# Kernel tuning notes

Measured on AMD Instinct MI355X. Metric: run time of the kernel, lower is better.

Reference implementation:

```python
import jax, jax.numpy as jnp
import numpy as np

VOCAB = 100000
E = 256      # embedding dim == projection dim (required by layer-axis concat)
H = 2048     # lstm hidden dim
P = 256      # projection dim
B, T = 8, 96
CELL_CLIP = 3.0
PROJ_CLIP = 3.0
NUM_LAYERS = 2


def setup_inputs() -> dict:
    key = jax.random.key(0)
    ks = jax.random.split(key, 8)
    tokens = jax.random.randint(ks[0], (B, T), 0, VOCAB, dtype=jnp.int32)
    mask = jnp.ones((B, T, 1), dtype=jnp.float32)
    embed_table = jax.random.normal(ks[1], (VOCAB + 1, E), dtype=jnp.float32) * 0.05
    # stacked LSTM weights: index 0=fwd L0, 1=fwd L1, 2=bwd L0, 3=bwd L1
    Wk = jax.random.normal(ks[2], (4, E, 4 * H), dtype=jnp.float32) * 0.02
    Wr = jax.random.normal(ks[3], (4, P, 4 * H), dtype=jnp.float32) * 0.02
    b = jnp.zeros((4, 4 * H), dtype=jnp.float32)
    Wp = jax.random.normal(ks[4], (4, H, P), dtype=jnp.float32) * 0.02
    elmo_w = jnp.zeros((NUM_LAYERS + 1,), dtype=jnp.float32)
    gamma = jnp.ones((1,), dtype=jnp.float32)
    return {"tokens": tokens, "mask": mask, "embed_table": embed_table,
            "Wk": Wk, "Wr": Wr, "b": b, "Wp": Wp,
            "elmo_w": elmo_w, "gamma": gamma}


def _lstm_proj(x, m, Wk, Wr, b, Wp, reverse):
    # x: [B,T,E], m: [B,T,1]. LSTM with cell clip, output projection, proj clip.
    if reverse:
        x = jnp.flip(x, 1)
        m = jnp.flip(m, 1)
    xs = jnp.swapaxes(x, 0, 1)                     # [T,B,E]
    ms = jnp.swapaxes(m, 0, 1)                     # [T,B,1]
    xW = jnp.einsum('tbe,ef->tbf', xs, Wk) + b     # precompute input gates [T,B,4H]

    def step(carry, inp):
        h, c = carry                               # h:[B,P], c:[B,H]
        zx, mt = inp
        z = zx + h @ Wr                            # [B,4H]
        i, f, g, o = jnp.split(z, 4, axis=-1)
        i = jax.nn.sigmoid(i)
        f = jax.nn.sigmoid(f)
        g = jnp.tanh(g)
        o = jax.nn.sigmoid(o)
        c_new = jnp.clip(f * c + i * g, -CELL_CLIP, CELL_CLIP)
        h_new = jnp.clip((o * jnp.tanh(c_new)) @ Wp, -PROJ_CLIP, PROJ_CLIP)
        keep = mt > 0
        h_new = jnp.where(keep, h_new, h)
        c_new = jnp.where(keep, c_new, c)
        return (h_new, c_new), h_new

    h0 = jnp.zeros((x.shape[0], Wp.shape[1]), x.dtype)
    c0 = jnp.zeros((x.shape[0], Wp.shape[0]), x.dtype)
    _, hs = jax.lax.scan(step, (h0, c0), (xW, ms))
    out = jnp.swapaxes(hs, 0, 1)                   # [B,T,P]
    if reverse:
        out = jnp.flip(out, 1)
    return out


def _elmo_layers(tokens, mask, embed_table, Wk, Wr, b, Wp):
    emb = embed_table[tokens]                      # [B,T,E]
    dir_outs = []
    for rev, base in ((False, 0), (True, 2)):
        inp = emb
        outs = []
        for l in range(NUM_LAYERS):
            out = _lstm_proj(inp, mask, Wk[base + l], Wr[base + l],
                             b[base + l], Wp[base + l], rev)
            inp = inp + out if l > 0 else out      # skip connection on layer > 0
            outs.append(inp)
        dir_outs.append(outs)
    fwd, bwd = dir_outs
    layers = [jnp.concatenate([emb, emb], -1)]
    layers += [jnp.concatenate([f, bb], -1) for f, bb in zip(fwd, bwd)]
    return jnp.stack(layers, axis=1)               # [B, L+1, T, 2P]


def reference(tokens, mask, embed_table, Wk, Wr, b, Wp, elmo_w, gamma):
    all_emb = _elmo_layers(tokens, mask, embed_table, Wk, Wr, b, Wp)
    m = mask[:, None, :, :]                        # [B,1,T,1]
    num = jnp.sum(mask, axis=(1, 2))[:, None]      # [B,1]
    xm = all_emb * m
    mean = jnp.sum(xm, axis=(2, 3)) / num          # [B,L+1]
    mean = mean[:, :, None, None]
    var = jnp.sum(((xm - mean) * m) ** 2, axis=(2, 3)) / num
    var = var[:, :, None, None]
    normed = (all_emb - mean) / jnp.sqrt(var + 1e-12)
    w = jax.nn.softmax(elmo_w)[None, :, None, None]
    weighted = jnp.sum(w * normed, axis=1) * gamma  # [B,T,2P]
    return weighted
```

## Files before the change

kernel.cpp:

```cpp
#include <hip/hip_runtime.h>
#include <hip/hip_bf16.h>

#define DEVFN __device__ __forceinline__

static constexpr size_t OFF_CTRS   = 0;
static constexpr size_t OFF_STATS  = 131328;
static constexpr size_t OFF_EW     = 131584;
static constexpr size_t OFF_MASK32 = 131840;
static constexpr size_t OFF_EMB    = 135168;
static constexpr size_t OFF_WPT    = 921600;
static constexpr size_t OFF_BIAS   = 9310208;
static constexpr size_t OFF_XW     = 9441280;
static constexpr size_t OFF_OUT0   = 59772928;
static constexpr size_t OFF_OUT1   = 61345792;
static constexpr size_t OFF_Y      = 62918656;
static constexpr size_t OFF_H      = 75501568;

template<int BF>
DEVFN float ldin(const void* p, size_t i) {
  if (BF) {
    unsigned short u = ((const unsigned short*)p)[i];
    return __uint_as_float(((unsigned)u) << 16);
  }
  return ((const float*)p)[i];
}
DEVFN float ldraw(const void* p, size_t i, int bf) {
  if (bf) {
    unsigned short u = ((const unsigned short*)p)[i];
    return __uint_as_float(((unsigned)u) << 16);
  }
  return ((const float*)p)[i];
}

DEVFN float sigm(float x) { return 1.f / (1.f + __expf(-x)); }
DEVFN float clip3(float x) { return fminf(fmaxf(x, -3.f), 3.f); }

DEVFN int detect_bf(const void* maskp) {
  return (((const unsigned*)maskp)[0] == 0x3F800000u) ? 0 : 1;
}

template<int BF>
__global__ void prep_k(const int* __restrict__ tokens, const void* __restrict__ maskp,
                       const void* __restrict__ et, const void* __restrict__ bias,
                       const void* __restrict__ ew, const void* __restrict__ gm,
                       const void* __restrict__ Wp,
                       float* bias32, float* mask32, float* ew32, float* emb, float* WpT) {
  if (detect_bf(maskp) != BF) return;
  const int bid = blockIdx.x, tid = threadIdx.x;

  if (bid < 132) {
    size_t i = (size_t)bid * 256 + tid;
    if (i >= 33540) return;
    if (i < 32768)       bias32[i] = ldin<BF>(bias, i);
    else if (i < 33536)  mask32[i - 32768] = ldin<BF>(maskp, i - 32768);
    else if (i < 33539)  ew32[i - 33536]   = ldin<BF>(ew, i - 33536);
    else                 ew32[3] = ldin<BF>(gm, 0);
    return;
  }

  if (bid < 644) {
    const int r = bid - 132;
    const int kt = r & 31, pt = (r >> 5) & 3, dl = r >> 7;
    __shared__ float tile[64][65];
    for (int it = 0; it < 4; ++it) {
      int lin = it * 1024 + tid * 4;
      int kk = lin >> 6, pp = lin & 63;
      size_t src = ((size_t)(dl * 2048 + kt * 64 + kk)) * 256 + pt * 64 + pp;
      float v0, v1, v2, v3;
      if (BF) {
        const unsigned short* sp = (const unsigned short*)Wp + src;
        v0 = __uint_as_float(((unsigned)sp[0]) << 16);
        v1 = __uint_as_float(((unsigned)sp[1]) << 16);
        v2 = __uint_as_float(((unsigned)sp[2]) << 16);
        v3 = __uint_as_float(((unsigned)sp[3]) << 16);
      } else {
        float4 v = *(const float4*)((const float*)Wp + src);
        v0 = v.x; v1 = v.y; v2 = v.z; v3 = v.w;
      }
      tile[pp + 0][kk] = v0; tile[pp + 1][kk] = v1; tile[pp + 2][kk] = v2; tile[pp + 3][kk] = v3;
    }
    __syncthreads();
    for (int it = 0; it < 4; ++it) {
      int lin = it * 1024 + tid * 4;
      int pr = lin >> 6, kc = lin & 63;
      float4 o;
      o.x = tile[pr][kc + 0]; o.y = tile[pr][kc + 1]; o.z = tile[pr][kc + 2]; o.w = tile[pr][kc + 3];
      *(float4*)(WpT + ((size_t)(dl * 256 + pt * 64 + pr)) * 2048 + kt * 64 + kc) = o;
    }
    return;
  }

  const int bt = bid - 644;
  const int tok = tokens[bt];
  emb[(size_t)bt * 256 + tid] = ldin<BF>(et, (size_t)tok * 256 + tid);
}

template<int BF>
__global__ __launch_bounds__(256) void xw_gemm_k(
    const void* __restrict__ maskp, const float* __restrict__ x_fwd, const float* __restrict__ x_bwd,
    const void* __restrict__ Wk, const float* __restrict__ bias32, float* __restrict__ xW, int layer) {
  if (detect_bf(maskp) != BF) return;
  const int nt = blockIdx.x, mt = blockIdx.y, dir = blockIdx.z;
  const int dl = dir * 2 + layer;
  const float* xb = dir ? x_bwd : x_fwd;
  const int tid = threadIdx.x;

  __shared__ float As[16][68];
  __shared__ float Bs[16][68];

  float acc[4][4] = {};
  const int tx = tid & 15, ty = tid >> 4;

  const int am = tid >> 2;
  const int ak = (tid & 3) * 4;
  const int m_glob = mt * 64 + am;
  const int t_ = m_glob >> 3, b_ = m_glob & 7;
  const int tau = dir ? (95 - t_) : t_;
  const float* arow = xb + ((size_t)(b_ * 96 + tau)) * 256;

  const int bk = tid >> 4, bn = (tid & 15) * 4;

  for (int kb = 0; kb < 256; kb += 16) {
    float4 av = *(const float4*)(arow + kb + ak);
    As[ak + 0][am] = av.x; As[ak + 1][am] = av.y; As[ak + 2][am] = av.z; As[ak + 3][am] = av.w;

    size_t bidx = ((size_t)dl * 256 + (kb + bk)) * 8192 + (size_t)nt * 64 + bn;
    float b0, b1, b2, b3;
    if (BF) {
      ushort4 uv = *(const ushort4*)((const unsigned short*)Wk + bidx);
      b0 = __uint_as_float(((unsigned)uv.x) << 16);
      b1 = __uint_as_float(((unsigned)uv.y) << 16);
      b2 = __uint_as_float(((unsigned)uv.z) << 16);
      b3 = __uint_as_float(((unsigned)uv.w) << 16);
    } else {
      float4 fv = *(const float4*)((const float*)Wk + bidx);
      b0 = fv.x; b1 = fv.y; b2 = fv.z; b3 = fv.w;
    }
    Bs[bk][bn + 0] = b0; Bs[bk][bn + 1] = b1; Bs[bk][bn + 2] = b2; Bs[bk][bn + 3] = b3;
    __syncthreads();

#pragma unroll
    for (int kk = 0; kk < 16; ++kk) {
      float a0 = As[kk][ty * 4 + 0], a1 = As[kk][ty * 4 + 1], a2 = As[kk][ty * 4 + 2], a3 = As[kk][ty * 4 + 3];
      float c0 = Bs[kk][tx * 4 + 0], c1 = Bs[kk][tx * 4 + 1], c2 = Bs[kk][tx * 4 + 2], c3 = Bs[kk][tx * 4 + 3];
      acc[0][0] = fmaf(a0, c0, acc[0][0]); acc[0][1] = fmaf(a0, c1, acc[0][1]);
      acc[0][2] = fmaf(a0, c2, acc[0][2]); acc[0][3] = fmaf(a0, c3, acc[0][3]);
      acc[1][0] = fmaf(a1, c0, acc[1][0]); acc[1][1] = fmaf(a1, c1, acc[1][1]);
      acc[1][2] = fmaf(a1, c2, acc[1][2]); acc[1][3] = fmaf(a1, c3, acc[1][3]);
      acc[2][0] = fmaf(a2, c0, acc[2][0]); acc[2][1] = fmaf(a2, c1, acc[2][1]);
      acc[2][2] = fmaf(a2, c2, acc[2][2]); acc[2][3] = fmaf(a2, c3, acc[2][3]);
      acc[3][0] = fmaf(a3, c0, acc[3][0]); acc[3][1] = fmaf(a3, c1, acc[3][1]);
      acc[3][2] = fmaf(a3, c2, acc[3][2]); acc[3][3] = fmaf(a3, c3, acc[3][3]);
    }
    __syncthreads();
  }

  const int n0 = nt * 64 + tx * 4;
#pragma unroll
  for (int i = 0; i < 4; ++i) {
    int m = mt * 64 + ty * 4 + i;
    int tt = m >> 3, bb = m & 7;
    float4 o;
    o.x = acc[i][0] + bias32[dl * 8192 + n0 + 0];
    o.y = acc[i][1] + bias32[dl * 8192 + n0 + 1];
    o.z = acc[i][2] + bias32[dl * 8192 + n0 + 2];
    o.w = acc[i][3] + bias32[dl * 8192 + n0 + 3];
    *(float4*)(xW + (size_t)((dir * 96 + tt) * 8 + bb) * 8192 + n0) = o;
  }
}


__global__ __launch_bounds__(256, 2) void scan_kernel(
    const float* __restrict__ xW, const void* __restrict__ WrRaw, const void* __restrict__ maskp,
    const float* __restrict__ WpT, const float* __restrict__ mask32,
    float* __restrict__ out, float* __restrict__ hbuf, float* __restrict__ ybuf,
    int* ctrs, int layer) {
  const int tid = threadIdx.x;
  const int w = blockIdx.x;
  const int dir = w >> 8;
  const int g = w & 255;
  const int dl = dir * 2 + layer;

  __shared__ __align__(16) float wr_s[256 * 32];
  __shared__ __align__(16) float h_lds[2048];
  __shared__ float4 wp4_s[512];
  __shared__ float4 zpart[288];
  __shared__ float  z_s[32 * 9];
  __shared__ __align__(16) float xw_s[256];
  __shared__ float  mask_s[768];
  __shared__ float  c_s[64];
  __shared__ float  red_s[8];

  int* base   = ctrs + (layer * 2 + dir) * 4096;
  int* aline  = base + (g >> 2) * 64;
  int* myline = base + (tid & 63) * 64;
  int ep = 0;
  const int bf = detect_bf(maskp);

  {
    const size_t wrbase = (size_t)dl * 256 * 8192;
    for (int i = tid; i < 8192; i += 256) {
      int k = i >> 5, col = i & 31;
      wr_s[i] = ldraw(WrRaw, wrbase + (size_t)k * 8192 + (size_t)(col >> 3) * 2048 + g * 8 + (col & 7), bf);
    }
    const float4* wrow = (const float4*)(WpT + ((size_t)(dl * 256 + g)) * 2048);
    for (int i = tid; i < 512; i += 256) wp4_s[i] = wrow[i];
    for (int i = tid; i < 768; i += 256) mask_s[i] = mask32[i];
  }
  if (tid < 64) c_s[tid] = 0.f;

  const int ks = tid >> 6, colq = (tid >> 3) & 7, lb = tid & 7;
  const float4* wr4 = (const float4*)wr_s;
  const float4* xw4 = (const float4*)xw_s;
  const int pb = tid >> 5, pcol = tid & 31;

  float xwv = xW[(size_t)((dir * 96 + 0) * 8 + pb) * 8192 + (pcol >> 3) * 2048 + g * 8 + (pcol & 7)];

  for (int t = 0; t < 96; ++t) {
    const int tau = dir ? (95 - t) : t;
    const float* h_cur = hbuf + ((size_t)(t * 2 + dir)) * 2048;
    float* h_nxt = hbuf + ((size_t)((t + 1) * 2 + dir)) * 2048;
    float* y_t   = ybuf + ((size_t)(t * 2 + dir)) * 16384;

    if (t == 0) {
      ((float4*)h_lds)[tid * 2 + 0] = make_float4(0.f, 0.f, 0.f, 0.f);
      ((float4*)h_lds)[tid * 2 + 1] = make_float4(0.f, 0.f, 0.f, 0.f);
    } else {
      ((float4*)h_lds)[tid * 2 + 0] = ((const float4*)h_cur)[tid * 2 + 0];
      ((float4*)h_lds)[tid * 2 + 1] = ((const float4*)h_cur)[tid * 2 + 1];
    }
    __syncthreads();

    {
      float4 acc = make_float4(0.f, 0.f, 0.f, 0.f);
#pragma unroll 16
      for (int i = 0; i < 64; ++i) {
        int k = (ks << 6) + i;
        float hv = h_lds[k * 8 + lb];
        float4 wv = wr4[k * 8 + colq];
        acc.x = fmaf(hv, wv.x, acc.x); acc.y = fmaf(hv, wv.y, acc.y);
        acc.z = fmaf(hv, wv.z, acc.z); acc.w = fmaf(hv, wv.w, acc.w);
      }
      zpart[(ks * 8 + colq) * 9 + lb] = acc;
      xw_s[tid] = xwv;
    }
    __syncthreads();

    ++ep;
    if (tid < 64) {
      {
        const int b3 = tid & 7, cq = tid >> 3;
        float4 z0 = zpart[(0 * 8 + cq) * 9 + b3];
        float4 z1 = zpart[(1 * 8 + cq) * 9 + b3];
        float4 z2 = zpart[(2 * 8 + cq) * 9 + b3];
        float4 z3 = zpart[(3 * 8 + cq) * 9 + b3];
        float4 xv = xw4[b3 * 8 + cq];
        z_s[(cq * 4 + 0) * 9 + b3] = z0.x + z1.x + z2.x + z3.x + xv.x;
        z_s[(cq * 4 + 1) * 9 + b3] = z0.y + z1.y + z2.y + z3.y + xv.y;
        z_s[(cq * 4 + 2) * 9 + b3] = z0.z + z1.z + z2.z + z3.z + xv.z;
        z_s[(cq * 4 + 3) * 9 + b3] = z0.w + z1.w + z2.w + z3.w + xv.w;
        const int cell = cq;
        float zi = z_s[(0  + cell) * 9 + b3];
        float zf = z_s[(8  + cell) * 9 + b3];
        float zg = z_s[(16 + cell) * 9 + b3];
        float zo = z_s[(24 + cell) * 9 + b3];
        float ig = sigm(zi), fg = sigm(zf), gg = tanhf(zg), og = sigm(zo);
        float cold = c_s[tid];
        float cc = clip3(fg * cold + ig * gg);
        float yv = og * tanhf(cc);
        float m = mask_s[b3 * 96 + tau];
        c_s[tid] = (m > 0.f) ? cc : cold;
        __hip_atomic_store(&y_t[b3 * 2048 + g * 8 + cell], yv, __ATOMIC_RELAXED, __HIP_MEMORY_SCOPE_AGENT);
      }
      asm volatile("s_waitcnt vmcnt(0)" ::: "memory");
      if (tid == 0)
        __hip_atomic_fetch_add(aline, 1, __ATOMIC_RELAXED, __HIP_MEMORY_SCOPE_AGENT);
      const int tgt = 4 * ep;
      int v = __hip_atomic_load(myline, __ATOMIC_RELAXED, __HIP_MEMORY_SCOPE_AGENT);
      while (!__all(v >= tgt)) {
        __builtin_amdgcn_s_sleep(1);
        v = __hip_atomic_load(myline, __ATOMIC_RELAXED, __HIP_MEMORY_SCOPE_AGENT);
      }
    }
    __syncthreads();

    {
      const int b = tid >> 5, kq = tid & 31;
      const float4* yb = (const float4*)y_t + b * 512;
      float s = 0.f;
#pragma unroll 8
      for (int i = 0; i < 16; ++i) {
        int k4 = i * 32 + kq;
        float4 yv = yb[k4];
        float4 wv = wp4_s[k4];
        s = fmaf(yv.x, wv.x, s); s = fmaf(yv.y, wv.y, s);
        s = fmaf(yv.z, wv.z, s); s = fmaf(yv.w, wv.w, s);
      }
      if (t < 95)
        xwv = xW[(size_t)((dir * 96 + (t + 1)) * 8 + pb) * 8192 + (pcol >> 3) * 2048 + g * 8 + (pcol & 7)];
      s += __shfl_down(s, 16, 32);
      s += __shfl_down(s, 8, 32);
      s += __shfl_down(s, 4, 32);
      s += __shfl_down(s, 2, 32);
      s += __shfl_down(s, 1, 32);
      if (kq == 0) red_s[b] = s;
    }
    __syncthreads();

    ++ep;
    if (tid < 64) {
      float hv = 0.f;
      if (tid < 8) {
        float hc = clip3(red_s[tid]);
        float m = mask_s[tid * 96 + tau];
        float hp = h_lds[g * 8 + tid];
        hv = (m > 0.f) ? hc : hp;
        __hip_atomic_store(&h_nxt[g * 8 + tid], hv, __ATOMIC_RELAXED, __HIP_MEMORY_SCOPE_AGENT);
      }
      asm volatile("s_waitcnt vmcnt(0)" ::: "memory");
      if (tid == 0)
        __hip_atomic_fetch_add(aline, 1, __ATOMIC_RELAXED, __HIP_MEMORY_SCOPE_AGENT);
      const int tgt = 4 * ep;
      int v = __hip_atomic_load(myline, __ATOMIC_RELAXED, __HIP_MEMORY_SCOPE_AGENT);
      while (!__all(v >= tgt)) {
        __builtin_amdgcn_s_sleep(1);
        v = __hip_atomic_load(myline, __ATOMIC_RELAXED, __HIP_MEMORY_SCOPE_AGENT);
      }
      if (tid < 8)
        out[(size_t)((dir * 8 + tid) * 96 + tau) * 256 + g] = hv;
    }
    __syncthreads();
  }
}

DEVFN float layer_val(int l, int b, int t, int f, const float* emb, const float* out0, const float* out1) {
  const int half = f >> 8, p = f & 255;
  if (l == 0) return emb[(size_t)(b * 96 + t) * 256 + p];
  const size_t o = ((size_t)((half * 8 + b) * 96 + t)) * 256 + p;
  float v = out0[o];
  if (l == 2) v += out1[o];
  return v;
}

__global__ void mixA_k(const float* emb, const float* out0, const float* out1,
                       const float* mask32, float* stats) {
  const int b = blockIdx.x / 3, l = blockIdx.x % 3;
  float s1 = 0.f, s2 = 0.f;
  for (int idx = threadIdx.x; idx < 96 * 512; idx += 256) {
    int t = idx >> 9, f = idx & 511;
    float v = layer_val(l, b, t, f, emb, out0, out1);
    float m = mask32[b * 96 + t];
    s1 += m * v; s2 += m * v * v;
  }
  for (int off = 32; off; off >>= 1) { s1 += __shfl_down(s1, off); s2 += __shfl_down(s2, off); }
  __shared__ float p1[4], p2[4];
  if ((threadIdx.x & 63) == 0) { p1[threadIdx.x >> 6] = s1; p2[threadIdx.x >> 6] = s2; }
  __syncthreads();
  if (threadIdx.x == 0) {
    float S1 = p1[0] + p1[1] + p1[2] + p1[3];
    float S2 = p2[0] + p2[1] + p2[2] + p2[3];
    float num = 0.f;
    for (int t = 0; t < 96; ++t) num += mask32[b * 96 + t];
    float mean = S1 / num;
    float var = S2 / num - 2.f * mean * mean + 512.f * mean * mean;
    stats[(b * 3 + l) * 2 + 0] = mean;
    stats[(b * 3 + l) * 2 + 1] = rsqrtf(var + 1e-12f);
  }
}

__global__ void mixB_k(const void* maskp, const float* emb, const float* out0, const float* out1,
                       const float* stats, const float* ew32, void* outp) {
  const int idx = blockIdx.x * 256 + threadIdx.x;
  const int b = idx / 49152;
  const int r = idx % 49152;
  const int t = r >> 9, f = r & 511;
  float w0 = ew32[0], w1 = ew32[1], w2 = ew32[2], gm = ew32[3];
  float mx = fmaxf(w0, fmaxf(w1, w2));
  float e0 = __expf(w0 - mx), e1 = __expf(w1 - mx), e2 = __expf(w2 - mx);
  float inv = 1.f / (e0 + e1 + e2);
  float wl[3] = {e0 * inv, e1 * inv, e2 * inv};
  float acc = 0.f;
#pragma unroll
  for (int l = 0; l < 3; ++l) {
    float v = layer_val(l, b, t, f, emb, out0, out1);
    acc += wl[l] * (v - stats[(b * 3 + l) * 2]) * stats[(b * 3 + l) * 2 + 1];
  }
  acc *= gm;
  if (detect_bf(maskp)) ((__hip_bfloat16*)outp)[idx] = __float2bfloat16(acc);
  else                  ((float*)outp)[idx] = acc;
}

extern "C" void kernel_launch(void* const* d_in, const int* in_sizes, int n_in,
                              void* d_out, int out_size, void* d_ws, size_t ws_size,
                              hipStream_t stream) {
  const int*  tokens = (const int*)d_in[0];
  const void* maskp  = d_in[1];
  const void* embt   = d_in[2];
  const void* Wk     = d_in[3];
  const void* WrRaw  = d_in[4];
  const void* bias   = d_in[5];
  const void* Wp     = d_in[6];
  const void* ew     = d_in[7];
  const void* gm     = d_in[8];

  char* ws = (char*)d_ws;
  int*   ctrs   = (int*)(ws + OFF_CTRS);
  float* stats  = (float*)(ws + OFF_STATS);
  float* ew32   = (float*)(ws + OFF_EW);
  float* mask32 = (float*)(ws + OFF_MASK32);
  float* emb    = (float*)(ws + OFF_EMB);
  float* wpt    = (float*)(ws + OFF_WPT);
  float* bias32 = (float*)(ws + OFF_BIAS);
  float* xW     = (float*)(ws + OFF_XW);
  float* out0   = (float*)(ws + OFF_OUT0);
  float* out1   = (float*)(ws + OFF_OUT1);
  float* ybuf   = (float*)(ws + OFF_Y);
  float* hbuf   = (float*)(ws + OFF_H);

  hipMemsetAsync(d_ws, 0, 131072, stream);

  prep_k<0><<<1412, 256, 0, stream>>>(tokens, maskp, embt, bias, ew, gm, Wp,
                                      bias32, mask32, ew32, emb, wpt);
  prep_k<1><<<1412, 256, 0, stream>>>(tokens, maskp, embt, bias, ew, gm, Wp,
                                      bias32, mask32, ew32, emb, wpt);

  xw_gemm_k<0><<<dim3(128, 12, 2), 256, 0, stream>>>(maskp, emb, emb, Wk, bias32, xW, 0);
  xw_gemm_k<1><<<dim3(128, 12, 2), 256, 0, stream>>>(maskp, emb, emb, Wk, bias32, xW, 0);

  int l0 = 0, l1 = 1;
  {
    void* args[] = {&xW, &WrRaw, &maskp, &wpt, &mask32, &out0, &hbuf, &ybuf, &ctrs, &l0};
    hipError_t e = hipLaunchCooperativeKernel((void*)scan_kernel, dim3(512), dim3(256), args, 0, stream);
    if (e != hipSuccess)
      scan_kernel<<<512, 256, 0, stream>>>(xW, WrRaw, maskp, wpt, mask32, out0, hbuf, ybuf, ctrs, 0);
  }

  float* x_fwd = out0;
  float* x_bwd = out0 + (size_t)8 * 96 * 256;
  xw_gemm_k<0><<<dim3(128, 12, 2), 256, 0, stream>>>(maskp, x_fwd, x_bwd, Wk, bias32, xW, 1);
  xw_gemm_k<1><<<dim3(128, 12, 2), 256, 0, stream>>>(maskp, x_fwd, x_bwd, Wk, bias32, xW, 1);

  {
    void* args[] = {&xW, &WrRaw, &maskp, &wpt, &mask32, &out1, &hbuf, &ybuf, &ctrs, &l1};
    hipError_t e = hipLaunchCooperativeKernel((void*)scan_kernel, dim3(512), dim3(256), args, 0, stream);
    if (e != hipSuccess)
      scan_kernel<<<512, 256, 0, stream>>>(xW, WrRaw, maskp, wpt, mask32, out1, hbuf, ybuf, ctrs, 1);
  }

  mixA_k<<<24, 256, 0, stream>>>(emb, out0, out1, mask32, stats);
  mixB_k<<<1536, 256, 0, stream>>>(maskp, emb, out0, out1, stats, ew32, d_out);
}
```

Measured before the change: 2.425 ms.

## Replace full barrier wait with per-chunk counter polling during projection

Instead of waiting for all workgroups to publish their gate outputs before starting the projection dot product, each wave now polls only the counters for the chunk of y it is about to consume, visiting chunks in a rotated order per workgroup. This lets projection work start as soon as partial data is ready, overlapping the grid-wide synchronization with computation. The next step's xW prefetch is also moved into shared memory, loaded by otherwise idle threads. In exchange the code issues more atomic loads and spin loops inside the inner loop, and its correctness depends on the relaxed memory ordering being sufficient.

```diff
diff --git a/kernel.cpp b/kernel.cpp
--- a/kernel.cpp
+++ b/kernel.cpp
@@ -209,12 +209,14 @@
   }
   if (tid < 64) c_s[tid] = 0.f;
 
+  {
+    const int bb = tid >> 5, cc = tid & 31;
+    xw_s[tid] = xW[(size_t)((dir * 96 + 0) * 8 + bb) * 8192 + (cc >> 3) * 2048 + g * 8 + (cc & 7)];
+  }
+
   const int ks = tid >> 6, colq = (tid >> 3) & 7, lb = tid & 7;
   const float4* wr4 = (const float4*)wr_s;
   const float4* xw4 = (const float4*)xw_s;
-  const int pb = tid >> 5, pcol = tid & 31;
-
-  float xwv = xW[(size_t)((dir * 96 + 0) * 8 + pb) * 8192 + (pcol >> 3) * 2048 + g * 8 + (pcol & 7)];
 
   for (int t = 0; t < 96; ++t) {
     const int tau = dir ? (95 - t) : t;
@@ -242,7 +244,6 @@
         acc.z = fmaf(hv, wv.z, acc.z); acc.w = fmaf(hv, wv.w, acc.w);
       }
       zpart[(ks * 8 + colq) * 9 + lb] = acc;
-      xw_s[tid] = xwv;
     }
     __syncthreads();
 
@@ -275,29 +276,45 @@
       asm volatile("s_waitcnt vmcnt(0)" ::: "memory");
       if (tid == 0)
         __hip_atomic_fetch_add(aline, 1, __ATOMIC_RELAXED, __HIP_MEMORY_SCOPE_AGENT);
-      const int tgt = 4 * ep;
-      int v = __hip_atomic_load(myline, __ATOMIC_RELAXED, __HIP_MEMORY_SCOPE_AGENT);
-      while (!__all(v >= tgt)) {
-        __builtin_amdgcn_s_sleep(1);
-        v = __hip_atomic_load(myline, __ATOMIC_RELAXED, __HIP_MEMORY_SCOPE_AGENT);
-      }
     }
     __syncthreads();
 
     {
       const int b = tid >> 5, kq = tid & 31;
+      const int lane = tid & 63;
+      const int roto = (g + ((tid >> 6) << 2)) & 15;
+      const int tgtA = 4 * ep;
+      if (t < 95 && tid >= 64 && tid < 192) {
+        const int j = (tid - 64) * 2;
+        const int bb = j >> 5, cc = j & 31;
+        float2 x2 = *(const float2*)(xW + (size_t)((dir * 96 + t + 1) * 8 + bb) * 8192 + (cc >> 3) * 2048 + g * 8 + (cc & 7));
+        xw_s[j] = x2.x; xw_s[j + 1] = x2.y;
+      }
       const float4* yb = (const float4*)y_t + b * 512;
       float s = 0.f;
-#pragma unroll 8
+      int v = 0x7fffffff;
+      if (lane < 4)
+        v = __hip_atomic_load(base + ((roto & 15) * 4 + lane) * 64, __ATOMIC_RELAXED, __HIP_MEMORY_SCOPE_AGENT);
       for (int i = 0; i < 16; ++i) {
-        int k4 = i * 32 + kq;
+        const int ic = (i + roto) & 15;
+        while (!__all(v >= tgtA)) {
+          __builtin_amdgcn_s_sleep(1);
+          if (lane < 4)
+            v = __hip_atomic_load(base + (ic * 4 + lane) * 64, __ATOMIC_RELAXED, __HIP_MEMORY_SCOPE_AGENT);
+        }
+        asm volatile("" ::: "memory");
+        const int k4 = ic * 32 + kq;
         float4 yv = yb[k4];
         float4 wv = wp4_s[k4];
+        if (i < 15) {
+          const int icn = (i + 1 + roto) & 15;
+          if (lane < 4)
+            v = __hip_atomic_load(base + (icn * 4 + lane) * 64, __ATOMIC_RELAXED, __HIP_MEMORY_SCOPE_AGENT);
+          else v = 0x7fffffff;
+        }
         s = fmaf(yv.x, wv.x, s); s = fmaf(yv.y, wv.y, s);
         s = fmaf(yv.z, wv.z, s); s = fmaf(yv.w, wv.w, s);
       }
-      if (t < 95)
-        xwv = xW[(size_t)((dir * 96 + (t + 1)) * 8 + pb) * 8192 + (pcol >> 3) * 2048 + g * 8 + (pcol & 7)];
       s += __shfl_down(s, 16, 32);
       s += __shfl_down(s, 8, 32);
       s += __shfl_down(s, 4, 32);
```

Result: slower. 2.917 ms (+20.3%).

## Fuse forward and backward scans into one block to overlap barrier latency

Applied to the files above, without the earlier changes.

Each of the 256 workgroups now processes both the forward and backward directions of the LSTM scan, interleaving their phases. A grid-wide barrier for one direction is started while work for the other direction is computed, so much of the spin-wait latency is hidden behind useful work. The grid shrinks from 512 to 256 blocks, and LDS use per block roughly doubles because both directions' weights are held. The xW prefetch is also moved to vectorized float2 loads into shared memory. In exchange, each block does twice the serial compute per step and there are more __syncthreads per step.

```diff
diff --git a/kernel.cpp b/kernel.cpp
--- a/kernel.cpp
+++ b/kernel.cpp
@@ -169,135 +169,196 @@
   }
 }
 
-
-__global__ __launch_bounds__(256, 2) void scan_kernel(
+DEVFN void arrive(int* aline, int tid) {
+  asm volatile("s_waitcnt vmcnt(0)" ::: "memory");
+  if (tid == 0)
+    __hip_atomic_fetch_add(aline, 1, __ATOMIC_RELAXED, __HIP_MEMORY_SCOPE_AGENT);
+}
+DEVFN void poll64(int* myline, int tgt) {
+  int v = __hip_atomic_load(myline, __ATOMIC_RELAXED, __HIP_MEMORY_SCOPE_AGENT);
+  while (!__all(v >= tgt)) {
+    __builtin_amdgcn_s_sleep(1);
+    v = __hip_atomic_load(myline, __ATOMIC_RELAXED, __HIP_MEMORY_SCOPE_AGENT);
+  }
+}
+
+__global__ __launch_bounds__(256, 1) void scan_kernel(
     const float* __restrict__ xW, const void* __restrict__ WrRaw, const void* __restrict__ maskp,
     const float* __restrict__ WpT, const float* __restrict__ mask32,
     float* __restrict__ out, float* __restrict__ hbuf, float* __restrict__ ybuf,
     int* ctrs, int layer) {
   const int tid = threadIdx.x;
-  const int w = blockIdx.x;
-  const int dir = w >> 8;
-  const int g = w & 255;
-  const int dl = dir * 2 + layer;
-
-  __shared__ __align__(16) float wr_s[256 * 32];
-  __shared__ __align__(16) float h_lds[2048];
-  __shared__ float4 wp4_s[512];
+  const int g = blockIdx.x;
+  const int dlf = layer, dlb = 2 + layer;
+
+  __shared__ __align__(16) float wr_f[256 * 32];
+  __shared__ __align__(16) float wr_b[256 * 32];
+  __shared__ __align__(16) float hf_lds[2048];
+  __shared__ __align__(16) float hb_lds[2048];
+  __shared__ float4 wpf_s[512];
+  __shared__ float4 wpb_s[512];
   __shared__ float4 zpart[288];
   __shared__ float  z_s[32 * 9];
-  __shared__ __align__(16) float xw_s[256];
+  __shared__ __align__(16) float xwf_s[256];
+  __shared__ __align__(16) float xwb_s[256];
   __shared__ float  mask_s[768];
-  __shared__ float  c_s[64];
+  __shared__ float  cf_s[64], cb_s[64];
   __shared__ float  red_s[8];
 
-  int* base   = ctrs + (layer * 2 + dir) * 4096;
-  int* aline  = base + (g >> 2) * 64;
-  int* myline = base + (tid & 63) * 64;
-  int ep = 0;
+  int* arena_f = ctrs + (layer * 2 + 0) * 4096;
+  int* arena_b = ctrs + (layer * 2 + 1) * 4096;
+  int* alf = arena_f + (g >> 2) * 64;
+  int* alb = arena_b + (g >> 2) * 64;
+  int* mlf = arena_f + (tid & 63) * 64;
+  int* mlb = arena_b + (tid & 63) * 64;
+  int epf = 0, epb = 0;
   const int bf = detect_bf(maskp);
 
   {
-    const size_t wrbase = (size_t)dl * 256 * 8192;
+    const size_t wbf = (size_t)dlf * 256 * 8192;
+    const size_t wbb = (size_t)dlb * 256 * 8192;
     for (int i = tid; i < 8192; i += 256) {
       int k = i >> 5, col = i & 31;
-      wr_s[i] = ldraw(WrRaw, wrbase + (size_t)k * 8192 + (size_t)(col >> 3) * 2048 + g * 8 + (col & 7), bf);
-    }
-    const float4* wrow = (const float4*)(WpT + ((size_t)(dl * 256 + g)) * 2048);
-    for (int i = tid; i < 512; i += 256) wp4_s[i] = wrow[i];
+      size_t off = (size_t)k * 8192 + (size_t)(col >> 3) * 2048 + g * 8 + (col & 7);
+      wr_f[i] = ldraw(WrRaw, wbf + off, bf);
+      wr_b[i] = ldraw(WrRaw, wbb + off, bf);
+    }
+    const float4* wrf = (const float4*)(WpT + ((size_t)(dlf * 256 + g)) * 2048);
+    const float4* wrb = (const float4*)(WpT + ((size_t)(dlb * 256 + g)) * 2048);
+    for (int i = tid; i < 512; i += 256) { wpf_s[i] = wrf[i]; wpb_s[i] = wrb[i]; }
     for (int i = tid; i < 768; i += 256) mask_s[i] = mask32[i];
   }
-  if (tid < 64) c_s[tid] = 0.f;
+  if (tid < 64) { cf_s[tid] = 0.f; cb_s[tid] = 0.f; }
+  {
+    const int bb2 = tid >> 5, cc = tid & 31;
+    xwf_s[tid] = xW[(size_t)((0 * 96 + 0) * 8 + bb2) * 8192 + (cc >> 3) * 2048 + g * 8 + (cc & 7)];
+    xwb_s[tid] = xW[(size_t)((1 * 96 + 0) * 8 + bb2) * 8192 + (cc >> 3) * 2048 + g * 8 + (cc & 7)];
+  }
+  {
+    float4 z4 = make_float4(0.f, 0.f, 0.f, 0.f);
+    ((float4*)hf_lds)[tid * 2 + 0] = z4; ((float4*)hf_lds)[tid * 2 + 1] = z4;
+    ((float4*)hb_lds)[tid * 2 + 0] = z4; ((float4*)hb_lds)[tid * 2 + 1] = z4;
+  }
+  __syncthreads();
 
   const int ks = tid >> 6, colq = (tid >> 3) & 7, lb = tid & 7;
-  const float4* wr4 = (const float4*)wr_s;
-  const float4* xw4 = (const float4*)xw_s;
-  const int pb = tid >> 5, pcol = tid & 31;
-
-  float xwv = xW[(size_t)((dir * 96 + 0) * 8 + pb) * 8192 + (pcol >> 3) * 2048 + g * 8 + (pcol & 7)];
+  const float4* wr4f = (const float4*)wr_f;
+  const float4* wr4b = (const float4*)wr_b;
+  const float4* xw4f = (const float4*)xwf_s;
+  const float4* xw4b = (const float4*)xwb_s;
 
   for (int t = 0; t < 96; ++t) {
-    const int tau = dir ? (95 - t) : t;
-    const float* h_cur = hbuf + ((size_t)(t * 2 + dir)) * 2048;
-    float* h_nxt = hbuf + ((size_t)((t + 1) * 2 + dir)) * 2048;
-    float* y_t   = ybuf + ((size_t)(t * 2 + dir)) * 16384;
-
-    if (t == 0) {
-      ((float4*)h_lds)[tid * 2 + 0] = make_float4(0.f, 0.f, 0.f, 0.f);
-      ((float4*)h_lds)[tid * 2 + 1] = make_float4(0.f, 0.f, 0.f, 0.f);
-    } else {
-      ((float4*)h_lds)[tid * 2 + 0] = ((const float4*)h_cur)[tid * 2 + 0];
-      ((float4*)h_lds)[tid * 2 + 1] = ((const float4*)h_cur)[tid * 2 + 1];
-    }
-    __syncthreads();
+    const int tauf = t, taub = 95 - t;
+    float* yf  = ybuf + ((size_t)(t * 2 + 0)) * 16384;
+    float* yb_ = ybuf + ((size_t)(t * 2 + 1)) * 16384;
+    float* hnf = hbuf + ((size_t)((t + 1) * 2 + 0)) * 2048;
+    float* hnb = hbuf + ((size_t)((t + 1) * 2 + 1)) * 2048;
 
     {
       float4 acc = make_float4(0.f, 0.f, 0.f, 0.f);
 #pragma unroll 16
       for (int i = 0; i < 64; ++i) {
         int k = (ks << 6) + i;
-        float hv = h_lds[k * 8 + lb];
-        float4 wv = wr4[k * 8 + colq];
+        float hv = hf_lds[k * 8 + lb];
+        float4 wv = wr4f[k * 8 + colq];
         acc.x = fmaf(hv, wv.x, acc.x); acc.y = fmaf(hv, wv.y, acc.y);
         acc.z = fmaf(hv, wv.z, acc.z); acc.w = fmaf(hv, wv.w, acc.w);
       }
       zpart[(ks * 8 + colq) * 9 + lb] = acc;
-      xw_s[tid] = xwv;
-    }
-    __syncthreads();
-
-    ++ep;
+    }
+    __syncthreads();
+
+    ++epf;
     if (tid < 64) {
-      {
-        const int b3 = tid & 7, cq = tid >> 3;
-        float4 z0 = zpart[(0 * 8 + cq) * 9 + b3];
-        float4 z1 = zpart[(1 * 8 + cq) * 9 + b3];
-        float4 z2 = zpart[(2 * 8 + cq) * 9 + b3];
-        float4 z3 = zpart[(3 * 8 + cq) * 9 + b3];
-        float4 xv = xw4[b3 * 8 + cq];
-        z_s[(cq * 4 + 0) * 9 + b3] = z0.x + z1.x + z2.x + z3.x + xv.x;
-        z_s[(cq * 4 + 1) * 9 + b3] = z0.y + z1.y + z2.y + z3.y + xv.y;
-        z_s[(cq * 4 + 2) * 9 + b3] = z0.z + z1.z + z2.z + z3.z + xv.z;
-        z_s[(cq * 4 + 3) * 9 + b3] = z0.w + z1.w + z2.w + z3.w + xv.w;
-        const int cell = cq;
-        float zi = z_s[(0  + cell) * 9 + b3];
-        float zf = z_s[(8  + cell) * 9 + b3];
-        float zg = z_s[(16 + cell) * 9 + b3];
-        float zo = z_s[(24 + cell) * 9 + b3];
-        float ig = sigm(zi), fg = sigm(zf), gg = tanhf(zg), og = sigm(zo);
-        float cold = c_s[tid];
-        float cc = clip3(fg * cold + ig * gg);
-        float yv = og * tanhf(cc);
-        float m = mask_s[b3 * 96 + tau];
-        c_s[tid] = (m > 0.f) ? cc : cold;
-        __hip_atomic_store(&y_t[b3 * 2048 + g * 8 + cell], yv, __ATOMIC_RELAXED, __HIP_MEMORY_SCOPE_AGENT);
-      }
-      asm volatile("s_waitcnt vmcnt(0)" ::: "memory");
-      if (tid == 0)
-        __hip_atomic_fetch_add(aline, 1, __ATOMIC_RELAXED, __HIP_MEMORY_SCOPE_AGENT);
-      const int tgt = 4 * ep;
-      int v = __hip_atomic_load(myline, __ATOMIC_RELAXED, __HIP_MEMORY_SCOPE_AGENT);
-      while (!__all(v >= tgt)) {
-        __builtin_amdgcn_s_sleep(1);
-        v = __hip_atomic_load(myline, __ATOMIC_RELAXED, __HIP_MEMORY_SCOPE_AGENT);
-      }
+      const int b3 = tid & 7, cq = tid >> 3;
+      float4 z0 = zpart[(0 * 8 + cq) * 9 + b3];
+      float4 z1 = zpart[(1 * 8 + cq) * 9 + b3];
+      float4 z2 = zpart[(2 * 8 + cq) * 9 + b3];
+      float4 z3 = zpart[(3 * 8 + cq) * 9 + b3];
+      float4 xv = xw4f[b3 * 8 + cq];
+      z_s[(cq * 4 + 0) * 9 + b3] = z0.x + z1.x + z2.x + z3.x + xv.x;
+      z_s[(cq * 4 + 1) * 9 + b3] = z0.y + z1.y + z2.y + z3.y + xv.y;
+      z_s[(cq * 4 + 2) * 9 + b3] = z0.z + z1.z + z2.z + z3.z + xv.z;
+      z_s[(cq * 4 + 3) * 9 + b3] = z0.w + z1.w + z2.w + z3.w + xv.w;
+      const int cell = cq;
+      float zi = z_s[(0  + cell) * 9 + b3];
+      float zf = z_s[(8  + cell) * 9 + b3];
+      float zg = z_s[(16 + cell) * 9 + b3];
+      float zo = z_s[(24 + cell) * 9 + b3];
+      float ig = sigm(zi), fg = sigm(zf), gg = tanhf(zg), og = sigm(zo);
+      float cold = cf_s[tid];
+      float cc = clip3(fg * cold + ig * gg);
+      float yv = og * tanhf(cc);
+      float m = mask_s[b3 * 96 + tauf];
+      cf_s[tid] = (m > 0.f) ? cc : cold;
+      __hip_atomic_store(&yf[b3 * 2048 + g * 8 + cell], yv, __ATOMIC_RELAXED, __HIP_MEMORY_SCOPE_AGENT);
+      arrive(alf, tid);
     }
     __syncthreads();
 
     {
+      float4 acc = make_float4(0.f, 0.f, 0.f, 0.f);
+#pragma unroll 16
+      for (int i = 0; i < 64; ++i) {
+        int k = (ks << 6) + i;
+        float hv = hb_lds[k * 8 + lb];
+        float4 wv = wr4b[k * 8 + colq];
+        acc.x = fmaf(hv, wv.x, acc.x); acc.y = fmaf(hv, wv.y, acc.y);
+        acc.z = fmaf(hv, wv.z, acc.z); acc.w = fmaf(hv, wv.w, acc.w);
+      }
+      zpart[(ks * 8 + colq) * 9 + lb] = acc;
+    }
+    __syncthreads();
+
+    ++epb;
+    if (tid < 64) {
+      const int b3 = tid & 7, cq = tid >> 3;
+      float4 z0 = zpart[(0 * 8 + cq) * 9 + b3];
+      float4 z1 = zpart[(1 * 8 + cq) * 9 + b3];
+      float4 z2 = zpart[(2 * 8 + cq) * 9 + b3];
+      float4 z3 = zpart[(3 * 8 + cq) * 9 + b3];
+      float4 xv = xw4b[b3 * 8 + cq];
+      z_s[(cq * 4 + 0) * 9 + b3] = z0.x + z1.x + z2.x + z3.x + xv.x;
+      z_s[(cq * 4 + 1) * 9 + b3] = z0.y + z1.y + z2.y + z3.y + xv.y;
+      z_s[(cq * 4 + 2) * 9 + b3] = z0.z + z1.z + z2.z + z3.z + xv.z;
+      z_s[(cq * 4 + 3) * 9 + b3] = z0.w + z1.w + z2.w + z3.w + xv.w;
+      const int cell = cq;
+      float zi = z_s[(0  + cell) * 9 + b3];
+      float zf = z_s[(8  + cell) * 9 + b3];
+      float zg = z_s[(16 + cell) * 9 + b3];
+      float zo = z_s[(24 + cell) * 9 + b3];
+      float ig = sigm(zi), fg = sigm(zf), gg = tanhf(zg), og = sigm(zo);
+      float cold = cb_s[tid];
+      float cc = clip3(fg * cold + ig * gg);
+      float yv = og * tanhf(cc);
+      float m = mask_s[b3 * 96 + taub];
+      cb_s[tid] = (m > 0.f) ? cc : cold;
+      __hip_atomic_store(&yb_[b3 * 2048 + g * 8 + cell], yv, __ATOMIC_RELAXED, __HIP_MEMORY_SCOPE_AGENT);
+      arrive(alb, tid);
+    }
+    __syncthreads();
+
+    if (tid < 64) poll64(mlf, 4 * epf);
+    __syncthreads();
+
+    {
+      if (t < 95 && tid >= 64 && tid < 192) {
+        const int j = (tid - 64) * 2;
+        const int bb2 = j >> 5, cc = j & 31;
+        float2 x2 = *(const float2*)(xW + (size_t)((0 * 96 + t + 1) * 8 + bb2) * 8192 + (cc >> 3) * 2048 + g * 8 + (cc & 7));
+        xwf_s[j] = x2.x; xwf_s[j + 1] = x2.y;
+      }
       const int b = tid >> 5, kq = tid & 31;
-      const float4* yb = (const float4*)y_t + b * 512;
+      const float4* yb4 = (const float4*)yf + b * 512;
       float s = 0.f;
 #pragma unroll 8
       for (int i = 0; i < 16; ++i) {
         int k4 = i * 32 + kq;
-        float4 yv = yb[k4];
-        float4 wv = wp4_s[k4];
+        float4 yv = yb4[k4];
+        float4 wv = wpf_s[k4];
         s = fmaf(yv.x, wv.x, s); s = fmaf(yv.y, wv.y, s);
         s = fmaf(yv.z, wv.z, s); s = fmaf(yv.w, wv.w, s);
       }
-      if (t < 95)
-        xwv = xW[(size_t)((dir * 96 + (t + 1)) * 8 + pb) * 8192 + (pcol >> 3) * 2048 + g * 8 + (pcol & 7)];
       s += __shfl_down(s, 16, 32);
       s += __shfl_down(s, 8, 32);
       s += __shfl_down(s, 4, 32);
@@ -307,29 +368,73 @@
     }
     __syncthreads();
 
-    ++ep;
+    ++epf;
     if (tid < 64) {
       float hv = 0.f;
       if (tid < 8) {
         float hc = clip3(red_s[tid]);
-        float m = mask_s[tid * 96 + tau];
-        float hp = h_lds[g * 8 + tid];
+        float m = mask_s[tid * 96 + tauf];
+        float hp = hf_lds[g * 8 + tid];
         hv = (m > 0.f) ? hc : hp;
-        __hip_atomic_store(&h_nxt[g * 8 + tid], hv, __ATOMIC_RELAXED, __HIP_MEMORY_SCOPE_AGENT);
-      }
-      asm volatile("s_waitcnt vmcnt(0)" ::: "memory");
-      if (tid == 0)
-        __hip_atomic_fetch_add(aline, 1, __ATOMIC_RELAXED, __HIP_MEMORY_SCOPE_AGENT);
-      const int tgt = 4 * ep;
-      int v = __hip_atomic_load(myline, __ATOMIC_RELAXED, __HIP_MEMORY_SCOPE_AGENT);
-      while (!__all(v >= tgt)) {
-        __builtin_amdgcn_s_sleep(1);
-        v = __hip_atomic_load(myline, __ATOMIC_RELAXED, __HIP_MEMORY_SCOPE_AGENT);
-      }
+        __hip_atomic_store(&hnf[g * 8 + tid], hv, __ATOMIC_RELAXED, __HIP_MEMORY_SCOPE_AGENT);
+      }
+      arrive(alf, tid);
+      poll64(mlb, 4 * epb);
       if (tid < 8)
-        out[(size_t)((dir * 8 + tid) * 96 + tau) * 256 + g] = hv;
-    }
-    __syncthreads();
+        out[(size_t)((0 * 8 + tid) * 96 + tauf) * 256 + g] = hv;
+    }
+    __syncthreads();
+
+    {
+      if (t < 95 && tid >= 64 && tid < 192) {
+        const int j = (tid - 64) * 2;
+        const int bb2 = j >> 5, cc = j & 31;
+        float2 x2 = *(const float2*)(xW + (size_t)((1 * 96 + t + 1) * 8 + bb2) * 8192 + (cc >> 3) * 2048 + g * 8 + (cc & 7));
+        xwb_s[j] = x2.x; xwb_s[j + 1] = x2.y;
+      }
+      const int b = tid >> 5, kq = tid & 31;
+      const float4* yb4 = (const float4*)yb_ + b * 512;
+      float s = 0.f;
+#pragma unroll 8
+      for (int i = 0; i < 16; ++i) {
+        int k4 = i * 32 + kq;
+        float4 yv = yb4[k4];
+        float4 wv = wpb_s[k4];
+        s = fmaf(yv.x, wv.x, s); s = fmaf(yv.y, wv.y, s);
+        s = fmaf(yv.z, wv.z, s); s = fmaf(yv.w, wv.w, s);
+      }
+      s += __shfl_down(s, 16, 32);
+      s += __shfl_down(s, 8, 32);
+      s += __shfl_down(s, 4, 32);
+      s += __shfl_down(s, 2, 32);
+      s += __shfl_down(s, 1, 32);
+      if (kq == 0) red_s[b] = s;
+    }
+    __syncthreads();
+
+    ++epb;
+    if (tid < 64) {
+      float hv = 0.f;
+      if (tid < 8) {
+        float hc = clip3(red_s[tid]);
+        float m = mask_s[tid * 96 + taub];
+        float hp = hb_lds[g * 8 + tid];
+        hv = (m > 0.f) ? hc : hp;
+        __hip_atomic_store(&hnb[g * 8 + tid], hv, __ATOMIC_RELAXED, __HIP_MEMORY_SCOPE_AGENT);
+      }
+      arrive(alb, tid);
+      poll64(mlf, 4 * epf);
+      if (tid < 8)
+        out[(size_t)((1 * 8 + tid) * 96 + taub) * 256 + g] = hv;
+    }
+    __syncthreads();
+
+    ((float4*)hf_lds)[tid * 2 + 0] = ((const float4*)hnf)[tid * 2 + 0];
+    ((float4*)hf_lds)[tid * 2 + 1] = ((const float4*)hnf)[tid * 2 + 1];
+    if (tid < 64) poll64(mlb, 4 * epb);
+    __syncthreads();
+    ((float4*)hb_lds)[tid * 2 + 0] = ((const float4*)hnb)[tid * 2 + 0];
+    ((float4*)hb_lds)[tid * 2 + 1] = ((const float4*)hnb)[tid * 2 + 1];
   }
 }
 
@@ -430,9 +535,9 @@
   int l0 = 0, l1 = 1;
   {
     void* args[] = {&xW, &WrRaw, &maskp, &wpt, &mask32, &out0, &hbuf, &ybuf, &ctrs, &l0};
-    hipError_t e = hipLaunchCooperativeKernel((void*)scan_kernel, dim3(512), dim3(256), args, 0, stream);
+    hipError_t e = hipLaunchCooperativeKernel((void*)scan_kernel, dim3(256), dim3(256), args, 0, stream);
     if (e != hipSuccess)
-      scan_kernel<<<512, 256, 0, stream>>>(xW, WrRaw, maskp, wpt, mask32, out0, hbuf, ybuf, ctrs, 0);
+      scan_kernel<<<256, 256, 0, stream>>>(xW, WrRaw, maskp, wpt, mask32, out0, hbuf, ybuf, ctrs, 0);
   }
 
   float* x_fwd = out0;
@@ -442,9 +547,9 @@
 
   {
     void* args[] = {&xW, &WrRaw, &maskp, &wpt, &mask32, &out1, &hbuf, &ybuf, &ctrs, &l1};
-    hipError_t e = hipLaunchCooperativeKernel((void*)scan_kernel, dim3(512), dim3(256), args, 0, stream);
+    hipError_t e = hipLaunchCooperativeKernel((void*)scan_kernel, dim3(256), dim3(256), args, 0, stream);
     if (e != hipSuccess)
-      scan_kernel<<<512, 256, 0, stream>>>(xW, WrRaw, maskp, wpt, mask32, out1, hbuf, ybuf, ctrs, 1);
+      scan_kernel<<<256, 256, 0, stream>>>(xW, WrRaw, maskp, wpt, mask32, out1, hbuf, ybuf, ctrs, 1);
   }
 
   mixA_k<<<24, 256, 0, stream>>>(emb, out0, out1, mask32, stats);
```

Measured after the change: 2.298 ms. 1.06x faster.
